# Performance work log

Hardware: AMD Instinct MI355X
Metric: run time of the kernel (lower is better)

Reference implementation:

```python
import jax, jax.numpy as jnp
import numpy as np

B, S, ENC_D, DEC_D, ATTN_D, OUT_D = 32, 2048, 1024, 1024, 1024, 1024
SCALING = 1.0


def setup_inputs() -> dict:
    key = jax.random.key(0)
    ks = jax.random.split(key, 10)
    enc_states = jax.random.normal(ks[0], (B, S, ENC_D), dtype=jnp.float32)
    # lengths in [S//2, S] so every row has at least one valid position
    enc_len = jax.random.randint(ks[1], (B,), S // 2, S + 1, dtype=jnp.int32)
    dec_states = jax.random.normal(ks[2], (B, DEC_D), dtype=jnp.float32)
    s = 0.02
    W_enc = jax.random.normal(ks[3], (ENC_D, ATTN_D), dtype=jnp.float32) * s
    b_enc = jnp.zeros((ATTN_D,), dtype=jnp.float32)
    W_dec = jax.random.normal(ks[4], (DEC_D, ATTN_D), dtype=jnp.float32) * s
    b_dec = jnp.zeros((ATTN_D,), dtype=jnp.float32)
    w_attn = jax.random.normal(ks[5], (ATTN_D,), dtype=jnp.float32) * s
    W_out = jax.random.normal(ks[6], (ENC_D, OUT_D), dtype=jnp.float32) * s
    b_out = jnp.zeros((OUT_D,), dtype=jnp.float32)
    return {
        "enc_states": enc_states,
        "dec_states": dec_states,
        "W_enc": W_enc, "b_enc": b_enc,
        "W_dec": W_dec, "b_dec": b_dec,
        "w_attn": w_attn,
        "W_out": W_out, "b_out": b_out,
        "enc_len": enc_len,
    }


def reference(enc_states, dec_states, W_enc, b_enc, W_dec, b_dec, w_attn, W_out, b_out, enc_len):
    # precomputed_enc_h = mlp_enc(enc_states): [B, S, ATTN_D]
    enc_h = jnp.einsum("bse,ea->bsa", enc_states, W_enc) + b_enc
    # dec_h = mlp_dec(dec_states): [B, ATTN_D]
    dec_h = dec_states @ W_dec + b_dec
    # additive (Bahdanau) score: tanh(enc_h + dec_h) . w_attn -> [B, S]
    attn = jnp.einsum("bsa,a->bs", jnp.tanh(enc_h + dec_h[:, None, :]), w_attn)
    # length mask
    mask = jnp.arange(enc_states.shape[1])[None, :] < enc_len[:, None]  # [B, S]
    attn = jnp.where(mask, attn, -jnp.inf)
    attn = jax.nn.softmax(attn * SCALING, axis=-1)
    # context = attn @ enc_states -> [B, ENC_D]
    context = jnp.einsum("bs,bse->be", attn, enc_states)
    context = context @ W_out + b_out
    return (context, attn)
```

## Files before the change

kernel.cpp:

```cpp
#include <hip/hip_runtime.h>
#include <cstdint>
#include <cstddef>

#define BATCH 32
#define SEQ   2048
#define DIM   1024
#define MROWS (BATCH*SEQ)

typedef __attribute__((ext_vector_type(4))) float  floatx4;
typedef __attribute__((ext_vector_type(8))) short  short8;

__device__ __forceinline__ unsigned short f2bf(float f) {
  unsigned int u = __float_as_uint(f);
  u += 0x7fffu + ((u >> 16) & 1u);
  return (unsigned short)(u >> 16);
}

__device__ __forceinline__ void async16(const void* g, void* l) {
  __builtin_amdgcn_global_load_lds(
      (const __attribute__((address_space(1))) unsigned int*)g,
      (__attribute__((address_space(3))) unsigned int*)l, 16, 0, 0);
}

__device__ __forceinline__ float fast_tanh(float x) {
  float e = __expf(2.0f * x);
  return 1.0f - 2.0f * __builtin_amdgcn_rcpf(1.0f + e);
}

__global__ void k_prep(const float* __restrict__ enc, const int* __restrict__ enc_len,
                       unsigned short* __restrict__ Abf,
                       const float* __restrict__ W_enc, unsigned short* __restrict__ Wt,
                       const float* __restrict__ dec, const float* __restrict__ W_dec,
                       const float* __restrict__ b_dec, const float* __restrict__ b_enc,
                       float* __restrict__ dech) {
  int id = blockIdx.x;
  int tid = threadIdx.x;
  if (id < 8192) {
    int b = id >> 8;
    int r0 = (id & 255) * 8;
    if (r0 >= enc_len[b]) return;
    size_t base = ((size_t)b * SEQ + r0) * DIM;
    const float4* src = (const float4*)(enc + base);
    ushort4* dst = (ushort4*)(Abf + base);
#pragma unroll
    for (int i = 0; i < 8; ++i) {
      float4 v = src[tid + i * 256];
      ushort4 h;
      h.x = f2bf(v.x); h.y = f2bf(v.y); h.z = f2bf(v.z); h.w = f2bf(v.w);
      dst[tid + i * 256] = h;
    }
  } else if (id < 9216) {
    int t = id - 8192;
    int n0 = (t & 31) * 32, k0 = (t >> 5) * 32;
    __shared__ float tile[32][33];
    int tx = tid & 31, ty = tid >> 5;
#pragma unroll
    for (int i = 0; i < 4; ++i) {
      int y = ty + i * 8;
      tile[y][tx] = W_enc[(size_t)(k0 + y) * DIM + n0 + tx];
    }
    __syncthreads();
#pragma unroll
    for (int i = 0; i < 4; ++i) {
      int y = ty + i * 8;
      Wt[(size_t)(n0 + y) * DIM + k0 + tx] = f2bf(tile[tx][y]);
    }
  } else {
    int t = id - 9216;
    int x = t & 3, b = (t >> 2) & 31, z = t >> 7;
    int a = x * 256 + tid;
    float acc = (z == 0) ? (b_dec[a] + b_enc[a]) : 0.0f;
    const float* dr = dec + (size_t)b * DIM + z * 128;
    const float* wc = W_dec + (size_t)z * 128 * DIM + a;
#pragma unroll 8
    for (int e = 0; e < 128; ++e)
      acc = fmaf(dr[e], wc[(size_t)e * DIM], acc);
    atomicAdd(&dech[(size_t)b * DIM + a], acc);
  }
}

__global__ void __launch_bounds__(256, 2) k_gemm_bf16(
    const unsigned short* __restrict__ Abf,
    const unsigned short* __restrict__ Wt,
    const float* __restrict__ dech,
    const float* __restrict__ w_attn,
    const int* __restrict__ enc_len,
    float* __restrict__ score)
{
  int linear = blockIdx.x;
  int xcd = linear & 7;
  int j   = linear >> 3;
  int rb  = xcd * 32 + (j >> 3);
  int nb  = j & 7;

  int bb  = rb >> 3;
  int len = enc_len[bb];
  if (((rb & 7) * 256) >= len) return;

  __shared__ __align__(16) unsigned short sA[256 * 32];
  __shared__ __align__(16) unsigned short sB[128 * 32];

  int tid  = threadIdx.x;
  int w    = tid >> 6, lane = tid & 63;
  int wm   = (w >> 1) * 128, wn = (w & 1) * 64;
  int li   = lane & 15, g = lane >> 4;

  const unsigned short* Ab = Abf + (size_t)rb * 256 * DIM;
  const unsigned short* Bb = Wt  + (size_t)nb * 128 * DIM;

  floatx4 acc[8][4] = {};

  for (int kb = 0; kb < 32; ++kb) {
    __syncthreads();
#pragma unroll
    for (int i = 0; i < 4; ++i) {
      int seg = i * 4 + w;
      int p   = seg * 64 + lane;
      int row = p >> 2, q = p & 3;
      async16(Ab + (size_t)row * DIM + kb * 32 + q * 8, (char*)sA + seg * 1024);
    }
#pragma unroll
    for (int i = 0; i < 2; ++i) {
      int seg = i * 4 + w;
      int p   = seg * 64 + lane;
      int row = p >> 2, q = p & 3;
      async16(Bb + (size_t)row * DIM + kb * 32 + q * 8, (char*)sB + seg * 1024);
    }
    __syncthreads();

    short8 af[8], bfr[4];
#pragma unroll
    for (int t = 0; t < 8; ++t)
      af[t]  = *(const short8*)&sA[((wm + t * 16 + li) * 4 + g) * 8];
#pragma unroll
    for (int t = 0; t < 4; ++t)
      bfr[t] = *(const short8*)&sB[((wn + t * 16 + li) * 4 + g) * 8];
#pragma unroll
    for (int tm = 0; tm < 8; ++tm)
#pragma unroll
      for (int tn = 0; tn < 4; ++tn)
        acc[tm][tn] = __builtin_amdgcn_mfma_f32_16x16x32_bf16(af[tm], bfr[tn], acc[tm][tn], 0, 0, 0);
  }

  float dh[4], wa[4];
#pragma unroll
  for (int tn = 0; tn < 4; ++tn) {
    int n = nb * 128 + wn + tn * 16 + li;
    dh[tn] = dech[(size_t)bb * DIM + n];
    wa[tn] = w_attn[n];
  }
#pragma unroll
  for (int tm = 0; tm < 8; ++tm) {
    int mrow = rb * 256 + wm + tm * 16 + g * 4;
#pragma unroll
    for (int r = 0; r < 4; ++r) {
      float v = 0.0f;
#pragma unroll
      for (int tn = 0; tn < 4; ++tn)
        v = fmaf(wa[tn], fast_tanh(acc[tm][tn][r] + dh[tn]), v);
      v += __shfl_xor(v, 1);
      v += __shfl_xor(v, 2);
      v += __shfl_xor(v, 4);
      v += __shfl_xor(v, 8);
      if (li == 0) atomicAdd(&score[mrow + r], v);
    }
  }
}

__global__ void k_softmax(const float* __restrict__ score, const int* __restrict__ enc_len,
                          float* __restrict__ attn) {
  int b = blockIdx.x, tid = threadIdx.x;
  int len = enc_len[b];
  __shared__ float red[256];
  float v[8];
  float m = -1e30f;
#pragma unroll
  for (int i = 0; i < 8; ++i) {
    int s = tid + i * 256;
    v[i] = score[(size_t)b * SEQ + s];
    if (s < len) m = fmaxf(m, v[i]);
  }
  red[tid] = m; __syncthreads();
  for (int st = 128; st > 0; st >>= 1) {
    if (tid < st) red[tid] = fmaxf(red[tid], red[tid + st]);
    __syncthreads();
  }
  float mx = red[0]; __syncthreads();
  float sum = 0.0f;
#pragma unroll
  for (int i = 0; i < 8; ++i) {
    int s = tid + i * 256;
    float e = (s < len) ? __expf(v[i] - mx) : 0.0f;
    v[i] = e; sum += e;
  }
  red[tid] = sum; __syncthreads();
  for (int st = 128; st > 0; st >>= 1) {
    if (tid < st) red[tid] += red[tid + st];
    __syncthreads();
  }
  float inv = 1.0f / red[0];
#pragma unroll
  for (int i = 0; i < 8; ++i)
    attn[(size_t)b * SEQ + tid + i * 256] = v[i] * inv;
}

__global__ void k_context(const float* __restrict__ enc, const float* __restrict__ attn,
                          const int* __restrict__ enc_len, float* __restrict__ ctx) {
  int b = blockIdx.y, sc = blockIdx.x;
  int len = enc_len[b];
  int s0 = sc * 64;
  if (s0 >= len) return;
  int cnt = min(64, len - s0);
  int tid = threadIdx.x;
  const float* base = enc + ((size_t)b * SEQ + s0) * DIM + tid * 4;
  const float* ap   = attn + (size_t)b * SEQ + s0;
  float a0 = 0.f, a1 = 0.f, a2 = 0.f, a3 = 0.f;
  for (int i = 0; i < cnt; ++i) {
    float a = ap[i];
    float4 x = *(const float4*)(base + (size_t)i * DIM);
    a0 = fmaf(a, x.x, a0); a1 = fmaf(a, x.y, a1);
    a2 = fmaf(a, x.z, a2); a3 = fmaf(a, x.w, a3);
  }
  float* c = ctx + (size_t)b * DIM + tid * 4;
  atomicAdd(c + 0, a0); atomicAdd(c + 1, a1);
  atomicAdd(c + 2, a2); atomicAdd(c + 3, a3);
}

__global__ void k_out(const float* __restrict__ ctx, const float* __restrict__ W_out,
                      const float* __restrict__ b_out, float* __restrict__ out) {
  int b = blockIdx.y, z = blockIdx.z;
  int o = blockIdx.x * 256 + threadIdx.x;
  float acc = (z == 0) ? b_out[o] : 0.0f;
  const float* cr = ctx + (size_t)b * DIM + z * 128;
  const float* wc = W_out + (size_t)z * 128 * DIM + o;
#pragma unroll 8
  for (int e = 0; e < 128; ++e)
    acc = fmaf(cr[e], wc[(size_t)e * DIM], acc);
  atomicAdd(&out[(size_t)b * DIM + o], acc);
}

extern "C" void kernel_launch(void* const* d_in, const int* in_sizes, int n_in,
                              void* d_out, int out_size, void* d_ws, size_t ws_size,
                              hipStream_t stream) {
  (void)in_sizes; (void)n_in; (void)out_size; (void)ws_size;
  const float* enc_states = (const float*)d_in[0];
  const float* dec_states = (const float*)d_in[1];
  const float* W_enc      = (const float*)d_in[2];
  const float* b_enc      = (const float*)d_in[3];
  const float* W_dec      = (const float*)d_in[4];
  const float* b_dec      = (const float*)d_in[5];
  const float* w_attn     = (const float*)d_in[6];
  const float* W_out      = (const float*)d_in[7];
  const float* b_out      = (const float*)d_in[8];
  const int*   enc_len    = (const int*)  d_in[9];

  float* out_ctx  = (float*)d_out;
  float* out_attn = (float*)d_out + BATCH * DIM;

  char* ws = (char*)d_ws;
  unsigned short* Wt  = (unsigned short*)ws;
  float* score = (float*)(ws + (2u << 20));
  float* ctx   = (float*)(ws + (2u << 20) + 262144);
  float* dech  = (float*)(ws + (2u << 20) + 262144 + 131072);
  unsigned short* Abf = (unsigned short*)(ws + (3u << 20));

  hipMemsetAsync(ws + (2u << 20), 0, 262144 + 131072 + 131072, stream);
  hipMemsetAsync(d_out, 0, (size_t)BATCH * DIM * sizeof(float), stream);

  k_prep<<<10240, 256, 0, stream>>>(enc_states, enc_len, Abf, W_enc, Wt,
                                    dec_states, W_dec, b_dec, b_enc, dech);
  k_gemm_bf16<<<2048, 256, 0, stream>>>(Abf, Wt, dech, w_attn, enc_len, score);
  k_softmax<<<BATCH, 256, 0, stream>>>(score, enc_len, out_attn);
  k_context<<<dim3(32, BATCH), 256, 0, stream>>>(enc_states, out_attn, enc_len, ctx);
  k_out<<<dim3(4, BATCH, 8), 256, 0, stream>>>(ctx, W_out, b_out, out_ctx);
}
```

Before: 629.2 us.

## Fuse fp32-to-bf16 conversion of encoder states into the score GEMM A-tile load

Result: slower. 663.4 us (+5.4%).

```diff
diff --git a/kernel.cpp b/kernel.cpp
--- a/kernel.cpp
+++ b/kernel.cpp
@@ -16,6 +16,12 @@
   return (unsigned short)(u >> 16);
 }
 
+__device__ __forceinline__ unsigned int pack2(float lo, float hi) {
+  unsigned int a = __float_as_uint(lo) + 0x8000u;
+  unsigned int b = __float_as_uint(hi) + 0x8000u;
+  return __builtin_amdgcn_perm(b, a, 0x07060302u);
+}
+
 __device__ __forceinline__ void async16(const void* g, void* l) {
   __builtin_amdgcn_global_load_lds(
       (const __attribute__((address_space(1))) unsigned int*)g,
@@ -27,31 +33,14 @@
   return 1.0f - 2.0f * __builtin_amdgcn_rcpf(1.0f + e);
 }
 
-__global__ void k_prep(const float* __restrict__ enc, const int* __restrict__ enc_len,
-                       unsigned short* __restrict__ Abf,
-                       const float* __restrict__ W_enc, unsigned short* __restrict__ Wt,
+__global__ void k_prep(const float* __restrict__ W_enc, unsigned short* __restrict__ Wt,
                        const float* __restrict__ dec, const float* __restrict__ W_dec,
                        const float* __restrict__ b_dec, const float* __restrict__ b_enc,
-                       float* __restrict__ dech) {
+                       float* __restrict__ dech, float* __restrict__ out_ctx) {
   int id = blockIdx.x;
   int tid = threadIdx.x;
-  if (id < 8192) {
-    int b = id >> 8;
-    int r0 = (id & 255) * 8;
-    if (r0 >= enc_len[b]) return;
-    size_t base = ((size_t)b * SEQ + r0) * DIM;
-    const float4* src = (const float4*)(enc + base);
-    ushort4* dst = (ushort4*)(Abf + base);
-#pragma unroll
-    for (int i = 0; i < 8; ++i) {
-      float4 v = src[tid + i * 256];
-      ushort4 h;
-      h.x = f2bf(v.x); h.y = f2bf(v.y); h.z = f2bf(v.z); h.w = f2bf(v.w);
-      dst[tid + i * 256] = h;
-    }
-  } else if (id < 9216) {
-    int t = id - 8192;
-    int n0 = (t & 31) * 32, k0 = (t >> 5) * 32;
+  if (id < 1024) {
+    int n0 = (id & 31) * 32, k0 = (id >> 5) * 32;
     __shared__ float tile[32][33];
     int tx = tid & 31, ty = tid >> 5;
 #pragma unroll
@@ -65,8 +54,8 @@
       int y = ty + i * 8;
       Wt[(size_t)(n0 + y) * DIM + k0 + tx] = f2bf(tile[tx][y]);
     }
-  } else {
-    int t = id - 9216;
+  } else if (id < 2048) {
+    int t = id - 1024;
     int x = t & 3, b = (t >> 2) & 31, z = t >> 7;
     int a = x * 256 + tid;
     float acc = (z == 0) ? (b_dec[a] + b_enc[a]) : 0.0f;
@@ -76,11 +65,17 @@
     for (int e = 0; e < 128; ++e)
       acc = fmaf(dr[e], wc[(size_t)e * DIM], acc);
     atomicAdd(&dech[(size_t)b * DIM + a], acc);
-  }
-}
-
-__global__ void __launch_bounds__(256, 2) k_gemm_bf16(
-    const unsigned short* __restrict__ Abf,
+  } else {
+    int t = id - 2048;
+    float4* p = (float4*)out_ctx;
+#pragma unroll
+    for (int i = 0; i < 8; ++i)
+      p[(t * 256 + tid) * 8 + i] = make_float4(0.f, 0.f, 0.f, 0.f);
+  }
+}
+
+__global__ void __launch_bounds__(256, 2) k_gemm(
+    const float* __restrict__ A,
     const unsigned short* __restrict__ Wt,
     const float* __restrict__ dech,
     const float* __restrict__ w_attn,
@@ -90,56 +85,71 @@
   int linear = blockIdx.x;
   int xcd = linear & 7;
   int j   = linear >> 3;
-  int rb  = xcd * 32 + (j >> 3);
+  int rb  = xcd * 64 + (j >> 3);
   int nb  = j & 7;
 
-  int bb  = rb >> 3;
+  int bb  = rb >> 4;
   int len = enc_len[bb];
-  if (((rb & 7) * 256) >= len) return;
-
-  __shared__ __align__(16) unsigned short sA[256 * 32];
-  __shared__ __align__(16) unsigned short sB[128 * 32];
+  if (((rb & 15) * 128) >= len) return;
+
+  __shared__ __align__(16) unsigned short sA[128 * 64];
+  __shared__ __align__(16) unsigned short sB[128 * 64];
 
   int tid  = threadIdx.x;
   int w    = tid >> 6, lane = tid & 63;
-  int wm   = (w >> 1) * 128, wn = (w & 1) * 64;
+  int wm   = (w >> 1) * 64, wn = (w & 1) * 64;
   int li   = lane & 15, g = lane >> 4;
 
-  const unsigned short* Ab = Abf + (size_t)rb * 256 * DIM;
-  const unsigned short* Bb = Wt  + (size_t)nb * 128 * DIM;
-
-  floatx4 acc[8][4] = {};
-
-  for (int kb = 0; kb < 32; ++kb) {
+  const float*          Ab = A  + (size_t)rb * 128 * DIM;
+  const unsigned short* Bb = Wt + (size_t)nb * 128 * DIM;
+
+  floatx4 acc[4][4] = {};
+
+  for (int kb = 0; kb < 16; ++kb) {
     __syncthreads();
 #pragma unroll
     for (int i = 0; i < 4; ++i) {
       int seg = i * 4 + w;
       int p   = seg * 64 + lane;
-      int row = p >> 2, q = p & 3;
-      async16(Ab + (size_t)row * DIM + kb * 32 + q * 8, (char*)sA + seg * 1024);
-    }
-#pragma unroll
-    for (int i = 0; i < 2; ++i) {
-      int seg = i * 4 + w;
-      int p   = seg * 64 + lane;
-      int row = p >> 2, q = p & 3;
-      async16(Bb + (size_t)row * DIM + kb * 32 + q * 8, (char*)sB + seg * 1024);
-    }
-    __syncthreads();
-
-    short8 af[8], bfr[4];
-#pragma unroll
-    for (int t = 0; t < 8; ++t)
-      af[t]  = *(const short8*)&sA[((wm + t * 16 + li) * 4 + g) * 8];
-#pragma unroll
-    for (int t = 0; t < 4; ++t)
-      bfr[t] = *(const short8*)&sB[((wn + t * 16 + li) * 4 + g) * 8];
-#pragma unroll
-    for (int tm = 0; tm < 8; ++tm)
-#pragma unroll
-      for (int tn = 0; tn < 4; ++tn)
-        acc[tm][tn] = __builtin_amdgcn_mfma_f32_16x16x32_bf16(af[tm], bfr[tn], acc[tm][tn], 0, 0, 0);
+      int row = p >> 3, qp = p & 7;
+      int ql  = qp ^ (row & 7);
+      async16(Bb + (size_t)row * DIM + kb * 64 + ql * 8, (char*)sB + seg * 1024);
+    }
+#pragma unroll
+    for (int i = 0; i < 4; ++i) {
+      int p   = tid + i * 256;
+      int row = p >> 3, qp = p & 7;
+      int ql  = qp ^ (row & 7);
+      const float* src = Ab + (size_t)row * DIM + kb * 64 + ql * 8;
+      float4 v0 = *(const float4*)src;
+      float4 v1 = *(const float4*)(src + 4);
+      int4 pk;
+      pk.x = (int)pack2(v0.x, v0.y);
+      pk.y = (int)pack2(v0.z, v0.w);
+      pk.z = (int)pack2(v1.x, v1.y);
+      pk.w = (int)pack2(v1.z, v1.w);
+      *(int4*)&sA[(size_t)p * 8] = pk;
+    }
+    __syncthreads();
+
+#pragma unroll
+    for (int h = 0; h < 2; ++h) {
+      short8 af[4], bfr[4];
+#pragma unroll
+      for (int t = 0; t < 4; ++t) {
+        int row = wm + t * 16 + li;
+        int ca  = row * 8 + ((h * 4 + g) ^ (row & 7));
+        af[t]   = *(const short8*)&sA[(size_t)ca * 8];
+        int n   = wn + t * 16 + li;
+        int cb  = n * 8 + ((h * 4 + g) ^ (n & 7));
+        bfr[t]  = *(const short8*)&sB[(size_t)cb * 8];
+      }
+#pragma unroll
+      for (int tm = 0; tm < 4; ++tm)
+#pragma unroll
+        for (int tn = 0; tn < 4; ++tn)
+          acc[tm][tn] = __builtin_amdgcn_mfma_f32_16x16x32_bf16(af[tm], bfr[tn], acc[tm][tn], 0, 0, 0);
+    }
   }
 
   float dh[4], wa[4];
@@ -150,8 +160,8 @@
     wa[tn] = w_attn[n];
   }
 #pragma unroll
-  for (int tm = 0; tm < 8; ++tm) {
-    int mrow = rb * 256 + wm + tm * 16 + g * 4;
+  for (int tm = 0; tm < 4; ++tm) {
+    int mrow = rb * 128 + wm + tm * 16 + g * 4;
 #pragma unroll
     for (int r = 0; r < 4; ++r) {
       float v = 0.0f;
@@ -262,14 +272,12 @@
   float* score = (float*)(ws + (2u << 20));
   float* ctx   = (float*)(ws + (2u << 20) + 262144);
   float* dech  = (float*)(ws + (2u << 20) + 262144 + 131072);
-  unsigned short* Abf = (unsigned short*)(ws + (3u << 20));
-
-  hipMemsetAsync(ws + (2u << 20), 0, 262144 + 131072 + 131072, stream);
-  hipMemsetAsync(d_out, 0, (size_t)BATCH * DIM * sizeof(float), stream);
-
-  k_prep<<<10240, 256, 0, stream>>>(enc_states, enc_len, Abf, W_enc, Wt,
-                                    dec_states, W_dec, b_dec, b_enc, dech);
-  k_gemm_bf16<<<2048, 256, 0, stream>>>(Abf, Wt, dech, w_attn, enc_len, score);
+
+  hipMemsetAsync(ws + (2u << 20), 0, 524288, stream);
+
+  k_prep<<<2052, 256, 0, stream>>>(W_enc, Wt, dec_states, W_dec, b_dec, b_enc,
+                                   dech, out_ctx);
+  k_gemm<<<4096, 256, 0, stream>>>(enc_states, Wt, dech, w_attn, enc_len, score);
   k_softmax<<<BATCH, 256, 0, stream>>>(score, enc_len, out_attn);
   k_context<<<dim3(32, BATCH), 256, 0, stream>>>(enc_states, out_attn, enc_len, ctx);
   k_out<<<dim3(4, BATCH, 8), 256, 0, stream>>>(ctx, W_out, b_out, out_ctx);
```
